# Optimization experiments

Hardware: AMD Instinct MI355X
Metric: run time of the kernel (lower is better)

## Reference

```python
import jax, jax.numpy as jnp
import numpy as np

N_NODES = 100000
N_EDGES = 1600000
D_IN = 50
HIDDEN = 128
N_CLASSES = 8


def setup_inputs() -> dict:
    key = jax.random.key(0)
    ks = jax.random.split(key, 8)
    x = jax.random.normal(ks[0], (N_NODES, D_IN), dtype=jnp.float32)
    edge_index = jax.random.randint(ks[1], (2, N_EDGES), 0, N_NODES, dtype=jnp.int64)
    s1 = 1.0 / np.sqrt(D_IN)
    s2 = 1.0 / np.sqrt(HIDDEN)
    return {
        "x": x,
        "edge_index": edge_index,
        "W1_l": jax.random.normal(ks[2], (D_IN, HIDDEN), dtype=jnp.float32) * s1,
        "W1_r": jax.random.normal(ks[3], (D_IN, HIDDEN), dtype=jnp.float32) * s1,
        "b1": jnp.zeros((HIDDEN,), dtype=jnp.float32),
        "W2_l": jax.random.normal(ks[4], (HIDDEN, N_CLASSES), dtype=jnp.float32) * s2,
        "W2_r": jax.random.normal(ks[5], (HIDDEN, N_CLASSES), dtype=jnp.float32) * s2,
        "b2": jnp.zeros((N_CLASSES,), dtype=jnp.float32),
    }


def _sage_conv(h, src, dst, n_nodes, W_l, W_r, b):
    # mean aggregation of neighbor messages src -> dst
    msg = h[src]                                                   # [E, d]
    agg = jax.ops.segment_sum(msg, dst, num_segments=n_nodes)      # [N, d]
    deg = jax.ops.segment_sum(jnp.ones((src.shape[0], 1), h.dtype), dst,
                              num_segments=n_nodes)                # [N, 1]
    agg = agg / jnp.maximum(deg, 1.0)
    # PyG SAGEConv: lin_l(aggregated) + lin_r(root), bias in lin_l
    return agg @ W_l + h @ W_r + b


def reference(x, edge_index, W1_l, W1_r, b1, W2_l, W2_r, b2):
    n_nodes = x.shape[0]
    src, dst = edge_index[0], edge_index[1]
    h = jax.nn.relu(_sage_conv(x, src, dst, n_nodes, W1_l, W1_r, b1))
    # dropout p=0.5 is identity in eval mode (deterministic baseline)
    return _sage_conv(h, src, dst, n_nodes, W2_l, W2_r, b2)
```

## Files before the change

kernel.cpp:

```cpp
#include <hip/hip_runtime.h>

#define N_NODES 100000
#define N_EDGES 1600000
#define D_IN    50
#define HIDDEN  128
#define NCLS    8

#define TILE    4096
#define NTILES  ((N_EDGES + TILE - 1) / TILE)
#define BSHIFT  9
#define NB      196

#define LW 68

typedef __bf16 bf16_t;
typedef bf16_t bf16x8 __attribute__((ext_vector_type(8)));
typedef float  f32x4  __attribute__((ext_vector_type(4)));

__device__ __forceinline__ unsigned f2bf(float f) {
    union { float f; unsigned u; } a; a.f = f;
    unsigned u = a.u;
    return (u + 0x7FFFu + ((u >> 16) & 1u)) >> 16;
}
__device__ __forceinline__ unsigned pack2(float a, float b) {
    return f2bf(a) | (f2bf(b) << 16);
}
__device__ __forceinline__ float bf_lo(unsigned v) { return __uint_as_float(v << 16); }
__device__ __forceinline__ float bf_hi(unsigned v) { return __uint_as_float(v & 0xFFFF0000u); }

__global__ __launch_bounds__(256) void conv_x_kernel(
    const float* __restrict__ x, unsigned* __restrict__ xb,
    unsigned* __restrict__ acat)
{
    int t = blockIdx.x * 256 + threadIdx.x;
    if (t >= N_NODES * 32) return;
    int n = t >> 5, j = t & 31;
    if (j < 25) {
        float2 v = ((const float2*)x)[n * 25 + j];
        unsigned pk = pack2(v.x, v.y);
        xb[n * 25 + j] = pk;
        acat[(size_t)n * 64 + 25 + j] = pk;
    } else {
        int z = n * 64 + 50 + (j - 25) * 2;
        acat[z] = 0u;
        acat[z + 1] = 0u;
    }
}

__global__ __launch_bounds__(256) void conv_w_kernel(
    const float* __restrict__ W1l, const float* __restrict__ W1r,
    const float* __restrict__ W2l, const float* __restrict__ W2r,
    unsigned* __restrict__ Wt1g, unsigned* __restrict__ W2tg)
{
    int t = blockIdx.x * 256 + threadIdx.x;
    if (t < 8192) {
        int n = t >> 6, kp = t & 63;
        int k0 = kp * 2, k1 = k0 + 1;
        float v0 = (k0 < 50) ? W1l[k0 * 128 + n] : ((k0 < 100) ? W1r[(k0 - 50) * 128 + n] : 0.0f);
        float v1 = (k1 < 50) ? W1l[k1 * 128 + n] : ((k1 < 100) ? W1r[(k1 - 50) * 128 + n] : 0.0f);
        Wt1g[t] = pack2(v0, v1);
    } else if (t < 8192 + 1024) {
        int u = t - 8192;
        int n2 = u >> 6, kp = u & 63;
        int k0 = kp * 2;
        float v0 = (n2 < 8) ? W2l[k0 * 8 + n2] : W2r[k0 * 8 + n2 - 8];
        float v1 = (n2 < 8) ? W2l[(k0 + 1) * 8 + n2] : W2r[(k0 + 1) * 8 + n2 - 8];
        W2tg[u] = pack2(v0, v1);
    }
}

__global__ __launch_bounds__(256) void passA_kernel(
    const int* __restrict__ dst, int* __restrict__ g_hist)
{
    __shared__ int lh[NB];
    int tid = threadIdx.x;
    for (int i = tid; i < NB; i += 256) lh[i] = 0;
    __syncthreads();
    int base = blockIdx.x * TILE;
    int cnt = min(TILE, N_EDGES - base);
    for (int i = tid; i < cnt; i += 256)
        atomicAdd(&lh[dst[base + i] >> BSHIFT], 1);
    __syncthreads();
    for (int i = tid; i < NB; i += 256) g_hist[blockIdx.x * NB + i] = lh[i];
}

__global__ __launch_bounds__(512) void passB_kernel(
    int* __restrict__ g_hist, int* __restrict__ btot)
{
    __shared__ int s[512];
    int b = blockIdx.x, tid = threadIdx.x;
    int v = (tid < NTILES) ? g_hist[tid * NB + b] : 0;
    s[tid] = v;
    __syncthreads();
    for (int d = 1; d < 512; d <<= 1) {
        int t = (tid >= d) ? s[tid - d] : 0;
        __syncthreads();
        s[tid] += t;
        __syncthreads();
    }
    if (tid < NTILES) g_hist[tid * NB + b] = s[tid] - v;
    if (tid == 511) btot[b] = s[511];
}

__global__ __launch_bounds__(256) void passB2_kernel(
    const int* __restrict__ btot, int* __restrict__ bbase, int* __restrict__ offs)
{
    __shared__ int s[256];
    int tid = threadIdx.x;
    int v = (tid < NB) ? btot[tid] : 0;
    s[tid] = v;
    __syncthreads();
    for (int d = 1; d < 256; d <<= 1) {
        int t = (tid >= d) ? s[tid - d] : 0;
        __syncthreads();
        s[tid] += t;
        __syncthreads();
    }
    if (tid < NB) bbase[tid] = s[tid] - v;
    if (tid == 0) offs[N_NODES] = N_EDGES;
}

__global__ __launch_bounds__(256) void passC_kernel(
    const int* __restrict__ src, const int* __restrict__ dst,
    const int* __restrict__ g_hist, const int* __restrict__ bbase,
    unsigned* __restrict__ bk_pack)
{
    __shared__ int hist[NB];
    __shared__ int seg[NB];
    __shared__ int cur[NB];
    __shared__ int gof[NB];
    __shared__ int sc[256];
    __shared__ unsigned s_pack[TILE];
    __shared__ unsigned short s_bkt[TILE];

    int tid = threadIdx.x, tile = blockIdx.x;
    int base = tile * TILE;
    int cnt = min(TILE, N_EDGES - base);

    for (int i = tid; i < NB; i += 256) {
        hist[i] = 0;
        gof[i] = g_hist[tile * NB + i] + bbase[i];
    }
    __syncthreads();

    int es[16], ed[16];
    #pragma unroll
    for (int k = 0; k < 16; ++k) {
        int i = tid + k * 256;
        if (i < cnt) {
            es[k] = src[base + i];
            ed[k] = dst[base + i];
            atomicAdd(&hist[ed[k] >> BSHIFT], 1);
        }
    }
    __syncthreads();

    {
        int v = (tid < NB) ? hist[tid] : 0;
        sc[tid] = v;
        __syncthreads();
        for (int d = 1; d < 256; d <<= 1) {
            int t = (tid >= d) ? sc[tid - d] : 0;
            __syncthreads();
            sc[tid] += t;
            __syncthreads();
        }
        if (tid < NB) { seg[tid] = sc[tid] - v; cur[tid] = sc[tid] - v; }
    }
    __syncthreads();

    #pragma unroll
    for (int k = 0; k < 16; ++k) {
        int i = tid + k * 256;
        if (i < cnt) {
            int b = ed[k] >> BSHIFT;
            int p = atomicAdd(&cur[b], 1);
            s_pack[p] = (unsigned)es[k] | ((unsigned)(ed[k] & 511) << 17);
            s_bkt[p] = (unsigned short)b;
        }
    }
    __syncthreads();

    for (int i = tid; i < cnt; i += 256) {
        int b = s_bkt[i];
        int g = gof[b] + (i - seg[b]);
        bk_pack[g] = s_pack[i];
    }
}

__global__ __launch_bounds__(512) void passD_kernel(
    const unsigned* __restrict__ bk_pack,
    const int* __restrict__ bbase, const int* __restrict__ btot,
    int* __restrict__ sorted_src, int* __restrict__ offs)
{
    __shared__ int ldeg[512];
    __shared__ int lofs[512];
    int b = blockIdx.x, tid = threadIdx.x;
    int ebase = bbase[b];
    int ecnt = btot[b];
    int nbase = b << BSHIFT;

    ldeg[tid] = 0;
    __syncthreads();
    for (int i = tid; i < ecnt; i += 512)
        atomicAdd(&ldeg[bk_pack[ebase + i] >> 17], 1);
    __syncthreads();

    int v = ldeg[tid];
    lofs[tid] = v;
    __syncthreads();
    for (int d = 1; d < 512; d <<= 1) {
        int t = (tid >= d) ? lofs[tid - d] : 0;
        __syncthreads();
        lofs[tid] += t;
        __syncthreads();
    }
    int ex = lofs[tid] - v;

    int node = nbase + tid;
    if (node < N_NODES) offs[node] = ebase + ex;

    ldeg[tid] = ex;
    __syncthreads();
    for (int i = tid; i < ecnt; i += 512) {
        unsigned pk = bk_pack[ebase + i];
        int p = atomicAdd(&ldeg[pk >> 17], 1);
        sorted_src[ebase + p] = (int)(pk & 0x1FFFFu);
    }
}

__global__ __launch_bounds__(256) void agg_x_kernel(
    const unsigned* __restrict__ xb,
    const int*      __restrict__ offs,
    const int*      __restrict__ ss,
    unsigned* __restrict__ acat)
{
    int node = blockIdx.x * 8 + (threadIdx.x >> 5);
    int dw   = threadIdx.x & 31;
    if (node >= N_NODES) return;
    int beg = offs[node], end = offs[node + 1];
    float2 a0 = {0.f,0.f}, a1 = {0.f,0.f}, a2 = {0.f,0.f}, a3 = {0.f,0.f};
    float2 a4 = {0.f,0.f}, a5 = {0.f,0.f}, a6 = {0.f,0.f}, a7 = {0.f,0.f};
    int i = beg;
    for (; i + 7 < end; i += 8) {
        int s0 = ss[i],     s1 = ss[i + 1], s2 = ss[i + 2], s3 = ss[i + 3];
        int s4 = ss[i + 4], s5 = ss[i + 5], s6 = ss[i + 6], s7 = ss[i + 7];
        if (dw < 25) {
            unsigned v0 = xb[s0 * 25 + dw];
            unsigned v1 = xb[s1 * 25 + dw];
            unsigned v2 = xb[s2 * 25 + dw];
            unsigned v3 = xb[s3 * 25 + dw];
            unsigned v4 = xb[s4 * 25 + dw];
            unsigned v5 = xb[s5 * 25 + dw];
            unsigned v6 = xb[s6 * 25 + dw];
            unsigned v7 = xb[s7 * 25 + dw];
            a0.x += bf_lo(v0); a0.y += bf_hi(v0);
            a1.x += bf_lo(v1); a1.y += bf_hi(v1);
            a2.x += bf_lo(v2); a2.y += bf_hi(v2);
            a3.x += bf_lo(v3); a3.y += bf_hi(v3);
            a4.x += bf_lo(v4); a4.y += bf_hi(v4);
            a5.x += bf_lo(v5); a5.y += bf_hi(v5);
            a6.x += bf_lo(v6); a6.y += bf_hi(v6);
            a7.x += bf_lo(v7); a7.y += bf_hi(v7);
        }
    }
    for (; i + 3 < end; i += 4) {
        int s0 = ss[i], s1 = ss[i + 1], s2 = ss[i + 2], s3 = ss[i + 3];
        if (dw < 25) {
            unsigned v0 = xb[s0 * 25 + dw];
            unsigned v1 = xb[s1 * 25 + dw];
            unsigned v2 = xb[s2 * 25 + dw];
            unsigned v3 = xb[s3 * 25 + dw];
            a0.x += bf_lo(v0); a0.y += bf_hi(v0);
            a1.x += bf_lo(v1); a1.y += bf_hi(v1);
            a2.x += bf_lo(v2); a2.y += bf_hi(v2);
            a3.x += bf_lo(v3); a3.y += bf_hi(v3);
        }
    }
    for (; i < end; ++i) {
        int s = ss[i];
        if (dw < 25) {
            unsigned v = xb[s * 25 + dw];
            a0.x += bf_lo(v); a0.y += bf_hi(v);
        }
    }
    if (dw < 25) {
        float inv = 1.0f / fmaxf((float)(end - beg), 1.0f);
        float sx = ((a0.x + a1.x) + (a2.x + a3.x)) + ((a4.x + a5.x) + (a6.x + a7.x));
        float sy = ((a0.y + a1.y) + (a2.y + a3.y)) + ((a4.y + a5.y) + (a6.y + a7.y));
        acat[(size_t)node * 64 + dw] = pack2(sx * inv, sy * inv);
    }
}

__global__ __launch_bounds__(256) void fused_mlp_kernel(
    const unsigned* __restrict__ Acat,
    const unsigned* __restrict__ Wt1g,
    const unsigned* __restrict__ W2tg,
    const float* __restrict__ b1,
    const float* __restrict__ b2,
    unsigned* __restrict__ pb,
    float* __restrict__ q)
{
    __shared__ unsigned sWt[128 * LW];
    __shared__ unsigned sW2t[16 * LW];
    __shared__ bf16_t   sH[4][16 * 136];

    int tid = threadIdx.x;
    for (int t = tid; t < 128 * 64; t += 256)
        sWt[(t >> 6) * LW + (t & 63)] = Wt1g[t];
    for (int t = tid; t < 16 * 64; t += 256)
        sW2t[(t >> 6) * LW + (t & 63)] = W2tg[t];
    __syncthreads();

    const int w    = tid >> 6;
    const int lane = tid & 63;
    const int lo   = lane & 15;
    const int g    = lane >> 4;

    float b1v[8][4];
    #pragma unroll
    for (int nt = 0; nt < 8; ++nt)
        #pragma unroll
        for (int r = 0; r < 4; ++r)
            b1v[nt][r] = b1[nt * 16 + g * 4 + r];
    float b2v[4];
    #pragma unroll
    for (int r = 0; r < 4; ++r)
        b2v[r] = (g >= 2) ? b2[(g - 2) * 4 + r] : 0.0f;

    bf16_t* myH = &sH[w][0];

    for (int tile = blockIdx.x; tile * 64 < N_NODES; tile += gridDim.x) {
        int node = tile * 64 + w * 16 + lo;
        int nclamp = min(node, N_NODES - 1);

        int4 bi[4];
        #pragma unroll
        for (int ks = 0; ks < 4; ++ks)
            bi[ks] = *((const int4*)(Acat + (size_t)nclamp * 64 + ks * 16 + g * 4));

        f32x4 acc[8];
        #pragma unroll
        for (int nt = 0; nt < 8; ++nt) acc[nt] = (f32x4)0.0f;
        #pragma unroll
        for (int nt = 0; nt < 8; ++nt) {
            #pragma unroll
            for (int ks = 0; ks < 4; ++ks) {
                int4 ai = *((const int4*)(sWt + (nt * 16 + lo) * LW + ks * 16 + g * 4));
                acc[nt] = __builtin_amdgcn_mfma_f32_16x16x32_bf16(
                    __builtin_bit_cast(bf16x8, ai),
                    __builtin_bit_cast(bf16x8, bi[ks]), acc[nt], 0, 0, 0);
            }
        }

        #pragma unroll
        for (int nt = 0; nt < 8; ++nt) {
            union { bf16_t h[4]; uint2 u; } pk;
            #pragma unroll
            for (int r = 0; r < 4; ++r)
                pk.h[r] = (bf16_t)fmaxf(acc[nt][r] + b1v[nt][r], 0.0f);
            *((uint2*)(myH + lo * 136 + nt * 16 + g * 4)) = pk.u;
        }
        __syncthreads();

        f32x4 acc2 = (f32x4)0.0f;
        #pragma unroll
        for (int ks = 0; ks < 4; ++ks) {
            int4 a2 = *((const int4*)(sW2t + lo * LW + ks * 16 + g * 4));
            int4 h2 = *((const int4*)(myH + lo * 136 + ks * 32 + g * 8));
            acc2 = __builtin_amdgcn_mfma_f32_16x16x32_bf16(
                __builtin_bit_cast(bf16x8, a2),
                __builtin_bit_cast(bf16x8, h2), acc2, 0, 0, 0);
        }

        if (node < N_NODES) {
            if (g < 2) {
                union { bf16_t h[4]; uint2 u; } pk;
                #pragma unroll
                for (int r = 0; r < 4; ++r) pk.h[r] = (bf16_t)acc2[r];
                *((uint2*)(pb + (size_t)node * 4 + g * 2)) = pk.u;
            } else {
                float4 qq;
                qq.x = acc2[0] + b2v[0];
                qq.y = acc2[1] + b2v[1];
                qq.z = acc2[2] + b2v[2];
                qq.w = acc2[3] + b2v[3];
                *((float4*)(q + (size_t)node * 8 + (g - 2) * 4)) = qq;
            }
        }
        __syncthreads();
    }
}

__global__ __launch_bounds__(256) void aggp_final_kernel(
    const unsigned* __restrict__ pb,
    const float*    __restrict__ q,
    const int*      __restrict__ offs,
    const int*      __restrict__ ss,
    float* __restrict__ out)
{
    int node = blockIdx.x * 4 + (threadIdx.x >> 6);
    int lane = threadIdx.x & 63;
    int k  = lane >> 2;
    int c2 = lane & 3;
    if (node >= N_NODES) return;
    int beg = offs[node], end = offs[node + 1];
    float2 acc = make_float2(0.0f, 0.0f);
    int i = beg + k;
    int sNext = (i < end) ? ss[i] : 0;
    for (; i < end; i += 16) {
        int s = sNext;
        int i2 = i + 16;
        sNext = (i2 < end) ? ss[i2] : 0;
        unsigned v = pb[s * 4 + c2];
        acc.x += bf_lo(v);
        acc.y += bf_hi(v);
    }
    acc.x += __shfl_xor(acc.x, 4);  acc.y += __shfl_xor(acc.y, 4);
    acc.x += __shfl_xor(acc.x, 8);  acc.y += __shfl_xor(acc.y, 8);
    acc.x += __shfl_xor(acc.x, 16); acc.y += __shfl_xor(acc.y, 16);
    acc.x += __shfl_xor(acc.x, 32); acc.y += __shfl_xor(acc.y, 32);
    if (lane < 4) {
        float inv = 1.0f / fmaxf((float)(end - beg), 1.0f);
        float2 qq = ((const float2*)(q + (size_t)node * NCLS))[c2];
        ((float2*)(out + (size_t)node * NCLS))[c2] =
            make_float2(acc.x * inv + qq.x, acc.y * inv + qq.y);
    }
}

extern "C" void kernel_launch(void* const* d_in, const int* in_sizes, int n_in,
                              void* d_out, int out_size, void* d_ws, size_t ws_size,
                              hipStream_t stream)
{
    const float* x   = (const float*)d_in[0];
    const int*   ei  = (const int*)  d_in[1];
    const float* W1l = (const float*)d_in[2];
    const float* W1r = (const float*)d_in[3];
    const float* b1  = (const float*)d_in[4];
    const float* W2l = (const float*)d_in[5];
    const float* W2r = (const float*)d_in[6];
    const float* b2  = (const float*)d_in[7];
    float* out = (float*)d_out;

    const int* src = ei;
    const int* dst = ei + N_EDGES;

    int* ws = (int*)d_ws;
    int*      offs       = ws;
    int*      g_hist     = offs + (N_NODES + 4);
    int*      btot       = g_hist + NTILES * NB;
    int*      bbase      = btot + 256;
    int*      sorted_src = bbase + 256;
    unsigned* xb         = (unsigned*)(sorted_src + N_EDGES);
    unsigned* Acat       = xb + (size_t)N_NODES * 25;
    unsigned* Wt1g       = Acat + (size_t)N_NODES * 64;
    unsigned* W2tg       = Wt1g + 8192;
    unsigned* pb         = W2tg + 1024;
    float*    q          = (float*)(pb + (size_t)N_NODES * 4);
    unsigned* bk_pack    = (unsigned*)(q + (size_t)N_NODES * 8);

    conv_x_kernel<<<(N_NODES * 32 + 255) / 256, 256, 0, stream>>>(x, xb, Acat);
    conv_w_kernel<<<36, 256, 0, stream>>>(W1l, W1r, W2l, W2r, Wt1g, W2tg);

    passA_kernel <<<NTILES, 256, 0, stream>>>(dst, g_hist);
    passB_kernel <<<NB, 512, 0, stream>>>(g_hist, btot);
    passB2_kernel<<<1, 256, 0, stream>>>(btot, bbase, offs);
    passC_kernel <<<NTILES, 256, 0, stream>>>(src, dst, g_hist, bbase, bk_pack);
    passD_kernel <<<NB, 512, 0, stream>>>(bk_pack, bbase, btot, sorted_src, offs);

    agg_x_kernel<<<(N_NODES + 7) / 8, 256, 0, stream>>>(xb, offs, sorted_src, Acat);

    fused_mlp_kernel<<<512, 256, 0, stream>>>(Acat, Wt1g, W2tg, b1, b2, pb, q);

    aggp_final_kernel<<<(N_NODES + 3) / 4, 256, 0, stream>>>(
        (const unsigned*)pb, q, offs, sorted_src, out);
}
```

Baseline: 133.9 us.

## Gather first-layer neighbor features as FP8 with two edges per half-wave

Stores a padded FP8 copy of x (64 bytes per node) and makes the layer-1 mean aggregation gather it instead of the bf16 copy. Each 32-lane group now handles two edges at once, each lane decoding four features, with a cross-half shuffle reduction at the end. This is meant to halve the random-gather bytes and the per-edge load count. In exchange it loses precision on the neighbor features (FP8 e4m3), which may hurt accuracy tolerance.

```diff
diff --git a/kernel.cpp b/kernel.cpp
--- a/kernel.cpp
+++ b/kernel.cpp
@@ -16,6 +16,7 @@
 typedef __bf16 bf16_t;
 typedef bf16_t bf16x8 __attribute__((ext_vector_type(8)));
 typedef float  f32x4  __attribute__((ext_vector_type(4)));
+typedef float  f32x2v __attribute__((ext_vector_type(2)));
 
 __device__ __forceinline__ unsigned f2bf(float f) {
     union { float f; unsigned u; } a; a.f = f;
@@ -29,21 +30,29 @@
 __device__ __forceinline__ float bf_hi(unsigned v) { return __uint_as_float(v & 0xFFFF0000u); }
 
 __global__ __launch_bounds__(256) void conv_x_kernel(
-    const float* __restrict__ x, unsigned* __restrict__ xb,
+    const float* __restrict__ x, unsigned* __restrict__ xb8,
     unsigned* __restrict__ acat)
 {
     int t = blockIdx.x * 256 + threadIdx.x;
     if (t >= N_NODES * 32) return;
     int n = t >> 5, j = t & 31;
+    const float2* x2 = (const float2*)x;
     if (j < 25) {
-        float2 v = ((const float2*)x)[n * 25 + j];
-        unsigned pk = pack2(v.x, v.y);
-        xb[n * 25 + j] = pk;
-        acat[(size_t)n * 64 + 25 + j] = pk;
+        float2 v = x2[n * 25 + j];
+        acat[(size_t)n * 64 + 25 + j] = pack2(v.x, v.y);
     } else {
         int z = n * 64 + 50 + (j - 25) * 2;
         acat[z] = 0u;
         acat[z + 1] = 0u;
+    }
+    if (j < 13) {
+        float2 u0 = x2[n * 25 + 2 * j];
+        float2 u1 = (j < 12) ? x2[n * 25 + 2 * j + 1] : make_float2(0.f, 0.f);
+        int w = __builtin_amdgcn_cvt_pk_fp8_f32(u0.x, u0.y, 0, false);
+        w = __builtin_amdgcn_cvt_pk_fp8_f32(u1.x, u1.y, w, true);
+        xb8[n * 16 + j] = (unsigned)w;
+    } else if (j >= 25 && j < 28) {
+        xb8[n * 16 + 13 + (j - 25)] = 0u;
     }
 }
 
@@ -229,66 +238,72 @@
     }
 }
 
+#define ACC8(a, v) { f32x2v lo_ = __builtin_amdgcn_cvt_pk_f32_fp8((v), false); \
+                     f32x2v hi_ = __builtin_amdgcn_cvt_pk_f32_fp8((v), true);  \
+                     a.x += lo_[0]; a.y += lo_[1]; a.z += hi_[0]; a.w += hi_[1]; }
+
 __global__ __launch_bounds__(256) void agg_x_kernel(
-    const unsigned* __restrict__ xb,
+    const unsigned* __restrict__ xb8,
     const int*      __restrict__ offs,
     const int*      __restrict__ ss,
     unsigned* __restrict__ acat)
 {
     int node = blockIdx.x * 8 + (threadIdx.x >> 5);
-    int dw   = threadIdx.x & 31;
+    int l32  = threadIdx.x & 31;
+    int slot = l32 >> 4;
+    int dw   = l32 & 15;
     if (node >= N_NODES) return;
     int beg = offs[node], end = offs[node + 1];
-    float2 a0 = {0.f,0.f}, a1 = {0.f,0.f}, a2 = {0.f,0.f}, a3 = {0.f,0.f};
-    float2 a4 = {0.f,0.f}, a5 = {0.f,0.f}, a6 = {0.f,0.f}, a7 = {0.f,0.f};
+    float4 a0 = {0,0,0,0}, a1 = {0,0,0,0}, a2 = {0,0,0,0}, a3 = {0,0,0,0};
+    float4 a4 = {0,0,0,0}, a5 = {0,0,0,0}, a6 = {0,0,0,0}, a7 = {0,0,0,0};
     int i = beg;
-    for (; i + 7 < end; i += 8) {
-        int s0 = ss[i],     s1 = ss[i + 1], s2 = ss[i + 2], s3 = ss[i + 3];
-        int s4 = ss[i + 4], s5 = ss[i + 5], s6 = ss[i + 6], s7 = ss[i + 7];
-        if (dw < 25) {
-            unsigned v0 = xb[s0 * 25 + dw];
-            unsigned v1 = xb[s1 * 25 + dw];
-            unsigned v2 = xb[s2 * 25 + dw];
-            unsigned v3 = xb[s3 * 25 + dw];
-            unsigned v4 = xb[s4 * 25 + dw];
-            unsigned v5 = xb[s5 * 25 + dw];
-            unsigned v6 = xb[s6 * 25 + dw];
-            unsigned v7 = xb[s7 * 25 + dw];
-            a0.x += bf_lo(v0); a0.y += bf_hi(v0);
-            a1.x += bf_lo(v1); a1.y += bf_hi(v1);
-            a2.x += bf_lo(v2); a2.y += bf_hi(v2);
-            a3.x += bf_lo(v3); a3.y += bf_hi(v3);
-            a4.x += bf_lo(v4); a4.y += bf_hi(v4);
-            a5.x += bf_lo(v5); a5.y += bf_hi(v5);
-            a6.x += bf_lo(v6); a6.y += bf_hi(v6);
-            a7.x += bf_lo(v7); a7.y += bf_hi(v7);
-        }
-    }
-    for (; i + 3 < end; i += 4) {
-        int s0 = ss[i], s1 = ss[i + 1], s2 = ss[i + 2], s3 = ss[i + 3];
-        if (dw < 25) {
-            unsigned v0 = xb[s0 * 25 + dw];
-            unsigned v1 = xb[s1 * 25 + dw];
-            unsigned v2 = xb[s2 * 25 + dw];
-            unsigned v3 = xb[s3 * 25 + dw];
-            a0.x += bf_lo(v0); a0.y += bf_hi(v0);
-            a1.x += bf_lo(v1); a1.y += bf_hi(v1);
-            a2.x += bf_lo(v2); a2.y += bf_hi(v2);
-            a3.x += bf_lo(v3); a3.y += bf_hi(v3);
-        }
-    }
-    for (; i < end; ++i) {
-        int s = ss[i];
-        if (dw < 25) {
-            unsigned v = xb[s * 25 + dw];
-            a0.x += bf_lo(v); a0.y += bf_hi(v);
-        }
-    }
-    if (dw < 25) {
+    for (; i + 15 < end; i += 16) {
+        int s0 = ss[i + slot];
+        int s1 = ss[i + slot + 2];
+        int s2 = ss[i + slot + 4];
+        int s3 = ss[i + slot + 6];
+        int s4 = ss[i + slot + 8];
+        int s5 = ss[i + slot + 10];
+        int s6 = ss[i + slot + 12];
+        int s7 = ss[i + slot + 14];
+        unsigned v0 = xb8[s0 * 16 + dw];
+        unsigned v1 = xb8[s1 * 16 + dw];
+        unsigned v2 = xb8[s2 * 16 + dw];
+        unsigned v3 = xb8[s3 * 16 + dw];
+        unsigned v4 = xb8[s4 * 16 + dw];
+        unsigned v5 = xb8[s5 * 16 + dw];
+        unsigned v6 = xb8[s6 * 16 + dw];
+        unsigned v7 = xb8[s7 * 16 + dw];
+        ACC8(a0, v0); ACC8(a1, v1); ACC8(a2, v2); ACC8(a3, v3);
+        ACC8(a4, v4); ACC8(a5, v5); ACC8(a6, v6); ACC8(a7, v7);
+    }
+    for (; i + 1 < end; i += 2) {
+        unsigned v = xb8[ss[i + slot] * 16 + dw];
+        ACC8(a0, v);
+    }
+    if (i < end && slot == 0) {
+        unsigned v = xb8[ss[i] * 16 + dw];
+        ACC8(a0, v);
+    }
+    float4 t;
+    t.x = ((a0.x + a1.x) + (a2.x + a3.x)) + ((a4.x + a5.x) + (a6.x + a7.x));
+    t.y = ((a0.y + a1.y) + (a2.y + a3.y)) + ((a4.y + a5.y) + (a6.y + a7.y));
+    t.z = ((a0.z + a1.z) + (a2.z + a3.z)) + ((a4.z + a5.z) + (a6.z + a7.z));
+    t.w = ((a0.w + a1.w) + (a2.w + a3.w)) + ((a4.w + a5.w) + (a6.w + a7.w));
+    t.x += __shfl_xor(t.x, 16);
+    t.y += __shfl_xor(t.y, 16);
+    t.z += __shfl_xor(t.z, 16);
+    t.w += __shfl_xor(t.w, 16);
+    if (slot == 0 && dw < 13) {
         float inv = 1.0f / fmaxf((float)(end - beg), 1.0f);
-        float sx = ((a0.x + a1.x) + (a2.x + a3.x)) + ((a4.x + a5.x) + (a6.x + a7.x));
-        float sy = ((a0.y + a1.y) + (a2.y + a3.y)) + ((a4.y + a5.y) + (a6.y + a7.y));
-        acat[(size_t)node * 64 + dw] = pack2(sx * inv, sy * inv);
+        if (dw < 12) {
+            uint2 o;
+            o.x = pack2(t.x * inv, t.y * inv);
+            o.y = pack2(t.z * inv, t.w * inv);
+            *((uint2*)(acat + (size_t)node * 64 + dw * 2)) = o;
+        } else {
+            acat[(size_t)node * 64 + 24] = pack2(t.x * inv, t.y * inv);
+        }
     }
 }
 
@@ -451,15 +466,15 @@
     int*      btot       = g_hist + NTILES * NB;
     int*      bbase      = btot + 256;
     int*      sorted_src = bbase + 256;
-    unsigned* xb         = (unsigned*)(sorted_src + N_EDGES);
-    unsigned* Acat       = xb + (size_t)N_NODES * 25;
+    unsigned* xb8        = (unsigned*)(sorted_src + N_EDGES);
+    unsigned* Acat       = xb8 + (size_t)N_NODES * 16;
     unsigned* Wt1g       = Acat + (size_t)N_NODES * 64;
     unsigned* W2tg       = Wt1g + 8192;
     unsigned* pb         = W2tg + 1024;
     float*    q          = (float*)(pb + (size_t)N_NODES * 4);
     unsigned* bk_pack    = (unsigned*)(q + (size_t)N_NODES * 8);
 
-    conv_x_kernel<<<(N_NODES * 32 + 255) / 256, 256, 0, stream>>>(x, xb, Acat);
+    conv_x_kernel<<<(N_NODES * 32 + 255) / 256, 256, 0, stream>>>(x, xb8, Acat);
     conv_w_kernel<<<36, 256, 0, stream>>>(W1l, W1r, W2l, W2r, Wt1g, W2tg);
 
     passA_kernel <<<NTILES, 256, 0, stream>>>(dst, g_hist);
@@ -468,7 +483,7 @@
     passC_kernel <<<NTILES, 256, 0, stream>>>(src, dst, g_hist, bbase, bk_pack);
     passD_kernel <<<NB, 512, 0, stream>>>(bk_pack, bbase, btot, sorted_src, offs);
 
-    agg_x_kernel<<<(N_NODES + 7) / 8, 256, 0, stream>>>(xb, offs, sorted_src, Acat);
+    agg_x_kernel<<<(N_NODES + 7) / 8, 256, 0, stream>>>(xb8, offs, sorted_src, Acat);
 
     fused_mlp_kernel<<<512, 256, 0, stream>>>(Acat, Wt1g, W2tg, b1, b2, pb, q);
 
```

Measured after the change: 139.6 us. 4.2% more time.
